# Optimization experiments

Measured on AMD Instinct MI355X. Metric: run time of the kernel, lower is better.

Reference implementation:

```python
import jax, jax.numpy as jnp
import numpy as np

B, T, D, L, H = 8, 1024, 768, 8, 12
BLOCK_SIZE = 4
HD = D // H


def setup_inputs() -> dict:
    key = jax.random.key(0)
    ks = jax.random.split(key, 10)
    sd = 0.02
    return {
        "x_init": jax.random.normal(ks[0], (B, T, D), jnp.float32),
        "attn_proj_w": jax.random.normal(ks[1], (L, D), jnp.float32) * sd,
        "mlp_proj_w": jax.random.normal(ks[2], (L, D), jnp.float32) * sd,
        "Wqkv": jax.random.normal(ks[3], (L, D, 3 * D), jnp.float32) * sd,
        "Wo": jax.random.normal(ks[4], (L, D, D), jnp.float32) * sd,
        "Wm1": jax.random.normal(ks[5], (L, D, 4 * D), jnp.float32) * sd,
        "Wm2": jax.random.normal(ks[6], (L, 4 * D, D), jnp.float32) * sd,
        "attn_scale": 1.0 + jax.random.normal(ks[7], (L, D), jnp.float32) * sd,
        "mlp_scale": 1.0 + jax.random.normal(ks[8], (L, D), jnp.float32) * sd,
        "ln_s": jnp.ones((L,), jnp.float32),
    }


def _rms_norm(x):
    # F.rms_norm with eps=None -> eps = finfo(dtype).eps
    eps = jnp.finfo(x.dtype).eps
    return x * jax.lax.rsqrt(jnp.mean(x * x, axis=-1, keepdims=True) + eps)


def _aggregate(V, q):
    # V: [n, B, T, D]; scalar-query depth attention (keys RMS-normed, values raw)
    K = _rms_norm(V)
    logits = jnp.einsum('d,nbtd->nbt', q, K)
    w = jax.nn.softmax(logits, axis=0)
    return jnp.einsum('nbt,nbtd->btd', w, V)


def _mha(x, wqkv, wo):
    # causal multi-head self-attention
    b, t, d = x.shape
    qkv = x @ wqkv                                   # [b, t, 3D]
    q, k, v = jnp.split(qkv, 3, axis=-1)
    q = q.reshape(b, t, H, HD)
    k = k.reshape(b, t, H, HD)
    v = v.reshape(b, t, H, HD)
    scores = jnp.einsum('bqhd,bkhd->bhqk', q, k) / np.sqrt(HD).astype(np.float32)
    mask = jnp.tril(jnp.ones((t, t), bool))
    scores = jnp.where(mask[None, None], scores, jnp.asarray(-1e30, scores.dtype))
    attn = jax.nn.softmax(scores, axis=-1)
    out = jnp.einsum('bhqk,bkhd->bqhd', attn, v).reshape(b, t, d)
    return out @ wo


def reference(x_init, attn_proj_w, mlp_proj_w, Wqkv, Wo, Wm1, Wm2,
              attn_scale, mlp_scale, ln_s):
    boundary_every = max(1, BLOCK_SIZE // 2)
    hist = [x_init]          # committed block representations
    partial = x_init         # intra-block partial accumulator
    for l in range(L):
        s = ln_s[l]
        V = jnp.stack(hist + [partial], axis=0)          # [n_hist+1, B, T, D]
        h = _aggregate(V, attn_proj_w[l])
        if l % boundary_every == 0:
            hist.append(partial)
            partial = jnp.zeros_like(partial)
        attn_out = _mha(_rms_norm(h) * s, Wqkv[l], Wo[l])
        partial = partial + attn_scale[l][None, None, :] * attn_out
        V2 = jnp.stack(hist + [partial], axis=0)
        h = _aggregate(V2, mlp_proj_w[l])
        mlp_out = jax.nn.gelu((_rms_norm(h) * s) @ Wm1[l]) @ Wm2[l]
        partial = partial + mlp_scale[l][None, None, :] * mlp_out
    return partial
```

## Files before the change

kernel.cpp:

```cpp
#include <hip/hip_runtime.h>
#include <hip/hip_bf16.h>
#include <math.h>
#include <stdint.h>

#define D_MODEL 768
#define T_SEQ   1024
#define B_BATCH 8
#define NHEAD   12
#define HDIM    64
#define NLAYER  8

typedef unsigned short u16;
typedef __attribute__((ext_vector_type(8))) short bf16x8;
typedef __attribute__((ext_vector_type(4))) float f32x4;
typedef __attribute__((ext_vector_type(4))) uint32_t u32x4;

static constexpr size_t BTD  = (size_t)B_BATCH * T_SEQ * D_MODEL;
static constexpr int    ROWS = B_BATCH * T_SEQ;
static constexpr float  EPSF = 1.1920928955078125e-07f;


__device__ __forceinline__ u16 f2bf(float x) {
    __hip_bfloat16 h = __float2bfloat16(x);
    return __builtin_bit_cast(u16, h);
}
__device__ __forceinline__ float bf2f(u16 u) {
    __hip_bfloat16 h = __builtin_bit_cast(__hip_bfloat16, u);
    return __bfloat162float(h);
}
__device__ __forceinline__ void split_bf(float x, u16& hi, u16& lo) {
    hi = f2bf(x);
    lo = f2bf(x - bf2f(hi));
}
__device__ __forceinline__ uint32_t cvt_pk_bf16(float a, float b) {
    uint32_t r;
    asm("v_cvt_pk_bf16_f32 %0, %1, %2" : "=v"(r) : "v"(a), "v"(b));
    return r;
}
__device__ __forceinline__ f32x4 mfma16(bf16x8 a, bf16x8 b, f32x4 c) {
    return __builtin_amdgcn_mfma_f32_16x16x32_bf16(a, b, c, 0, 0, 0);
}

__device__ __forceinline__ void gl_lds16(const void* g, void* l) {
    auto gp = reinterpret_cast<const __attribute__((address_space(1))) char*>(
        reinterpret_cast<uintptr_t>(g));
    auto lp = reinterpret_cast<__attribute__((address_space(3))) char*>(
        static_cast<uint32_t>(reinterpret_cast<uintptr_t>(l)));
    __builtin_amdgcn_global_load_lds(gp, lp, 16, 0, 0);
}

__device__ __forceinline__ float block_reduce_sum(float v, float* sbuf) {
    #pragma unroll
    for (int off = 32; off > 0; off >>= 1) v += __shfl_down(v, off);
    __syncthreads();
    if ((threadIdx.x & 63) == 0) sbuf[threadIdx.x >> 6] = v;
    __syncthreads();
    return sbuf[0] + sbuf[1] + sbuf[2] + sbuf[3];
}

__device__ __forceinline__ float gelu_fast(float x) {
    float z = 0.7978845608028654f * (x + 0.044715f * x * x * x);
    float e = __expf(2.f * z);
    return x - x / (e + 1.f);
}

template<int N>
__global__ __launch_bounds__(256)
void agg_norm_kernel(const float* __restrict__ v0, const float* __restrict__ v1,
                     const float* __restrict__ v2, const float* __restrict__ v3,
                     const float* __restrict__ v4,
                     const float* __restrict__ q,  const float* __restrict__ lns,
                     u16* __restrict__ xh) {
    __shared__ float sbuf[4];
    const float* V[5] = {v0, v1, v2, v3, v4};
    const size_t row = blockIdx.x;
    const int tid = threadIdx.x;

    float outv[3];
    if constexpr (N == 1) {
        #pragma unroll
        for (int j = 0; j < 3; ++j) outv[j] = v0[row * D_MODEL + tid + j * 256];
    } else {
        float qv[3];
        #pragma unroll
        for (int j = 0; j < 3; ++j) qv[j] = q[tid + j * 256];

        float vv[N][3];
        float logits[N];
        #pragma unroll
        for (int i = 0; i < N; ++i) {
            const float* vr = V[i] + row * D_MODEL;
            float ssq = 0.f, qd = 0.f;
            #pragma unroll
            for (int j = 0; j < 3; ++j) {
                float x = vr[tid + j * 256];
                vv[i][j] = x;
                ssq = fmaf(x, x, ssq);
                qd  = fmaf(qv[j], x, qd);
            }
            float S  = block_reduce_sum(ssq, sbuf);
            float Qd = block_reduce_sum(qd,  sbuf);
            logits[i] = Qd * rsqrtf(S * (1.f / 768.f) + EPSF);
        }
        float mx = logits[0];
        #pragma unroll
        for (int i = 1; i < N; ++i) mx = fmaxf(mx, logits[i]);
        float w[N];
        #pragma unroll
        for (int i = 0; i < N; ++i) w[i] = __expf(logits[i] - mx);
        w[0] *= 2.f;
        float wsum = 0.f;
        #pragma unroll
        for (int i = 0; i < N; ++i) wsum += w[i];
        float inv = 1.f / wsum;
        outv[0] = outv[1] = outv[2] = 0.f;
        #pragma unroll
        for (int i = 0; i < N; ++i) {
            float wi = w[i] * inv;
            #pragma unroll
            for (int j = 0; j < 3; ++j) outv[j] = fmaf(wi, vv[i][j], outv[j]);
        }
    }
    float ssq = 0.f;
    #pragma unroll
    for (int j = 0; j < 3; ++j) ssq = fmaf(outv[j], outv[j], ssq);
    float S2 = block_reduce_sum(ssq, sbuf);
    float scale = lns[0] * rsqrtf(S2 * (1.f / 768.f) + EPSF);
    #pragma unroll
    for (int j = 0; j < 3; ++j)
        xh[row * D_MODEL + tid + j * 256] = f2bf(outv[j] * scale);
}

__global__ __launch_bounds__(256)
void transpose_all(const float* __restrict__ Wqkv, const float* __restrict__ Wo,
                   const float* __restrict__ Wm1,  const float* __restrict__ Wm2,
                   u16* __restrict__ T0, u16* __restrict__ T1,
                   u16* __restrict__ T2, u16* __restrict__ T3) {
    const int id = blockIdx.x;
    const float* W; u16* Th; int K, N, t;
    if (id < 1728)      { W = Wqkv; Th = T0; K = 768;  N = 2304; t = id; }
    else if (id < 2304) { W = Wo;   Th = T1; K = 768;  N = 768;  t = id - 1728; }
    else if (id < 4608) { W = Wm1;  Th = T2; K = 768;  N = 3072; t = id - 2304; }
    else                { W = Wm2;  Th = T3; K = 3072; N = 768;  t = id - 4608; }
    const int nk = K >> 5;
    const int bk = (t % nk) * 32, bn = (t / nk) * 32;

    __shared__ float tt[32][33];
    const int r = threadIdx.x >> 3, c4 = (threadIdx.x & 7) * 4;
    float4 v = *(const float4*)&W[(size_t)(bk + r) * N + bn + c4];
    tt[r][c4 + 0] = v.x; tt[r][c4 + 1] = v.y; tt[r][c4 + 2] = v.z; tt[r][c4 + 3] = v.w;
    __syncthreads();
    u16 h[4];
    #pragma unroll
    for (int j = 0; j < 4; ++j) h[j] = f2bf(tt[c4 + j][r]);
    size_t o = (size_t)(bn + r) * K + bk + c4;
    *(uint2*)&Th[o] = make_uint2((uint32_t)h[0] | ((uint32_t)h[1] << 16),
                                 (uint32_t)h[2] | ((uint32_t)h[3] << 16));
}

__global__ __launch_bounds__(256)
void vt_transpose(const u16* __restrict__ vh, u16* __restrict__ vth) {
    __shared__ u16 th[32][36];
    const int bh = blockIdx.z;
    const int t0 = blockIdx.x * 32, d0 = blockIdx.y * 32;
    const int r = threadIdx.x >> 3, c = (threadIdx.x & 7) * 4;
    const size_t ib = ((size_t)(bh << 10) + t0 + r) * 64 + d0 + c;
    *(uint2*)&th[r][c] = *(const uint2*)&vh[ib];
    __syncthreads();
    const size_t ob = ((size_t)(bh << 6) + d0 + r) * 1024 + t0 + c;
    u16 a0 = th[c + 0][r], a1 = th[c + 1][r], a2 = th[c + 2][r], a3 = th[c + 3][r];
    *(uint2*)&vth[ob] = make_uint2((uint32_t)a0 | ((uint32_t)a1 << 16),
                                   (uint32_t)a2 | ((uint32_t)a3 << 16));
}

template<int EPI, int BN>
__global__ __launch_bounds__(256)
void gemm_bf1(const u16* __restrict__ Ah, const u16* __restrict__ Bh,
              float* __restrict__ Cf, u16* __restrict__ Ch,
              const float* __restrict__ scale, int M, int N, int K,
              u16* __restrict__ Qh, u16* __restrict__ Ql,
              u16* __restrict__ Kh, u16* __restrict__ Vh) {
    constexpr int NJ = BN / 32;
    constexpr int BUF_U16 = 4096 + BN * 32;
    __shared__ u16 smem[2 * BUF_U16];

    const int gx = gridDim.x, gy = gridDim.y;
    const int nwg = gx * gy;
    const int lin = blockIdx.y * gx + blockIdx.x;
    const int wg  = (lin & 7) * (nwg >> 3) + (lin >> 3);
    const int bn  = (wg % gx) * BN;
    const int bm  = (wg / gx) << 7;

    const int tid = threadIdx.x;
    const int w = tid >> 6, l = tid & 63;
    const int wr = w >> 1, wc = w & 1;

    const int grow = tid >> 2;
    const int gcol = (((tid & 3) ^ ((tid >> 3) & 3)) << 3);
    const size_t aoff0 = (size_t)(bm + grow) * K + gcol;
    const size_t boff0 = (size_t)(bn + grow) * K + gcol;
    const size_t s64 = (size_t)64 * K;
    char* sb0 = (char*)smem;
    char* sb1 = (char*)smem + 2 * BUF_U16;
    const uint32_t wq = (uint32_t)w << 10;

    auto stage = [&](char* sbuf, int k0) {
        gl_lds16(Ah + aoff0 + k0,       sbuf + 0    + wq);
        gl_lds16(Ah + aoff0 + s64 + k0, sbuf + 4096 + wq);
        gl_lds16(Bh + boff0 + k0,       sbuf + 8192 + wq);
        if constexpr (BN == 128)
            gl_lds16(Bh + boff0 + s64 + k0, sbuf + 12288 + wq);
    };

    f32x4 acc[4][NJ] = {};

    const int key8 = (((l & 15) >> 1) & 3) << 3;
    const int kswz = ((l >> 4) << 3) ^ key8;
    const int arow = wr * 64 + (l & 15);
    const int brow = wc * (BN / 2) + (l & 15);
    const int nk = K >> 5;

    stage(sb0, 0);
    for (int kt = 0; kt < nk; ++kt) {
        char* cur = (kt & 1) ? sb1 : sb0;
        char* nxt = (kt & 1) ? sb0 : sb1;
        if (kt + 1 < nk) {
            stage(nxt, (kt + 1) << 5);
            if constexpr (BN == 128)
                asm volatile("s_waitcnt vmcnt(4)\n\ts_barrier" ::: "memory");
            else
                asm volatile("s_waitcnt vmcnt(3)\n\ts_barrier" ::: "memory");
        } else {
            asm volatile("s_waitcnt vmcnt(0)\n\ts_barrier" ::: "memory");
        }
        __builtin_amdgcn_sched_barrier(0);

        const u16* bu = (const u16*)cur;
        bf16x8 ah[4], bh4[NJ];
        #pragma unroll
        for (int i = 0; i < 4; ++i)
            ah[i] = *(const bf16x8*)&bu[(arow + i * 16) * 32 + kswz];
        #pragma unroll
        for (int j = 0; j < NJ; ++j)
            bh4[j] = *(const bf16x8*)&bu[4096 + (brow + j * 16) * 32 + kswz];
        asm volatile("s_waitcnt lgkmcnt(0)" ::: "memory");
        __builtin_amdgcn_sched_barrier(0);
        asm volatile("s_barrier" ::: "memory");

        #pragma unroll
        for (int i = 0; i < 4; ++i) {
            #pragma unroll
            for (int j = 0; j < NJ; ++j)
                acc[i][j] = mfma16(ah[i], bh4[j], acc[i][j]);
        }
    }

    const int crow0 = bm + wr * 64 + ((l >> 4) << 2);
    const int ccol0 = bn + wc * (BN / 2) + (l & 15);
    #pragma unroll
    for (int i = 0; i < 4; ++i) {
        #pragma unroll
        for (int j = 0; j < NJ; ++j) {
            const int col = ccol0 + j * 16;
            #pragma unroll
            for (int r = 0; r < 4; ++r) {
                const int row = crow0 + i * 16 + r;
                const size_t o = (size_t)row * N + col;
                float v = acc[i][j][r];
                if (EPI == 1) {
                    Ch[o] = f2bf(gelu_fast(v));
                } else if (EPI == 2) {
                    Cf[o] += scale[col] * v;
                } else if (EPI == 4) {
                    Cf[o] = scale[col] * v;
                } else if (EPI == 3) {
                    const int which = (col >= 1536) ? 2 : ((col >= 768) ? 1 : 0);
                    const int hcol = col - which * 768;
                    const size_t dst = ((size_t)((row >> 10) * NHEAD + (hcol >> 6)) * 1024
                                        + (row & 1023)) * 64 + (hcol & 63);
                    if (which == 0) {
                        v *= 0.125f;
                        u16 hi, lo;
                        split_bf(v, hi, lo);
                        Qh[dst] = hi; Ql[dst] = lo;
                    } else if (which == 1) {
                        Kh[dst] = f2bf(v);
                    } else {
                        Vh[dst] = f2bf(v);
                    }
                }
            }
        }
    }
}

__global__ __launch_bounds__(256, 3)
void flash16(const u16* __restrict__ qh, const u16* __restrict__ ql,
             const u16* __restrict__ kh, const u16* __restrict__ vth,
             u16* __restrict__ ch) {
    const int id = blockIdx.x;
    const int r8 = id & 7, s = id >> 3;
    const int bh = r8 + 8 * (s >> 3);
    const int p  = s & 7;
    const int hh = bh % NHEAD, bb = bh / NHEAD;
    const int tid = threadIdx.x, w = tid >> 6, l = tid & 63;
    const int lq = l & 15, lg = l >> 4;
    const size_t hb = (size_t)bh << 16;

    const int wqA = p * 64 + w * 16;
    const int wqB = (15 - p) * 64 + w * 16;
    const int qA = wqA + lq, qB = wqB + lq;

    bf16x8 qA0, qA1, qA2, qA3, qB0, qB1, qB2, qB3;
    {
        const size_t qa = hb + ((size_t)qA << 6) + lg * 8;
        qA0 = *(const bf16x8*)(qh + qa);       qA1 = *(const bf16x8*)(ql + qa);
        qA2 = *(const bf16x8*)(qh + qa + 32);  qA3 = *(const bf16x8*)(ql + qa + 32);
        const size_t qb = hb + ((size_t)qB << 6) + lg * 8;
        qB0 = *(const bf16x8*)(qh + qb);       qB1 = *(const bf16x8*)(ql + qb);
        qB2 = *(const bf16x8*)(qh + qb + 32);  qB3 = *(const bf16x8*)(ql + qb + 32);
    }

    f32x4 oA[4] = {}, oB[4] = {};
    float mA = -30000.f, lsA = 0.f, mB = -30000.f, lsB = 0.f;
    const int ntiles = 32 - 2 * p;
    const int src0 = 32 * (lg & 1) + lq, src1 = src0 + 16;
    const bool hiHalf = lg >= 2;

    bf16x8 KA[4], KB[4], VA[4], VB[4];
    auto loadK = [&](bf16x8 (&K)[4], int k0) {
        const size_t kb0 = hb + (size_t)(k0 + lq) * 64 + lg * 8;
        const size_t kb1 = kb0 + 16 * 64;
        K[0] = *(const bf16x8*)(kh + kb0);
        K[1] = *(const bf16x8*)(kh + kb0 + 32);
        K[2] = *(const bf16x8*)(kh + kb1);
        K[3] = *(const bf16x8*)(kh + kb1 + 32);
    };
    auto loadV = [&](bf16x8 (&V)[4], int k0) {
        #pragma unroll
        for (int dt = 0; dt < 4; ++dt) {
            const size_t vb = hb + (size_t)(dt * 16 + lq) * 1024 + k0 + lg * 8;
            V[dt] = *(const bf16x8*)(vth + vb);
        }
    };

    auto path = [&](bf16x8 (&Kc)[4], bf16x8 (&vf)[4], int k0, int wqX, int qX,
                    bf16x8 q0, bf16x8 q1, bf16x8 q2, bf16x8 q3,
                    float& mX, float& lsX, f32x4 (&oX)[4]) {
        f32x4 s0 = {}, s1 = {};
        s0 = mfma16(Kc[0], q0, s0); s0 = mfma16(Kc[0], q1, s0);
        s0 = mfma16(Kc[1], q2, s0); s0 = mfma16(Kc[1], q3, s0);
        s1 = mfma16(Kc[2], q0, s1); s1 = mfma16(Kc[2], q1, s1);
        s1 = mfma16(Kc[3], q2, s1); s1 = mfma16(Kc[3], q3, s1);
        if (k0 + 31 > wqX) {
            #pragma unroll
            for (int r = 0; r < 4; ++r) {
                if (k0 + 4 * lg + r > qX)      s0[r] = -30000.f;
                if (k0 + 16 + 4 * lg + r > qX) s1[r] = -30000.f;
            }
        }
        float tmloc = fmaxf(fmaxf(fmaxf(s0[0], s0[1]), fmaxf(s0[2], s0[3])),
                            fmaxf(fmaxf(s1[0], s1[1]), fmaxf(s1[2], s1[3])));
        if (__any(tmloc > mX + 8.f)) {
            float tm = fmaxf(tmloc, __shfl_xor(tmloc, 16));
            tm = fmaxf(tm, __shfl_xor(tm, 32));
            const float mnew = fmaxf(mX, tm);
            const float fac = __expf(mX - mnew);
            mX = mnew;
            lsX *= fac;
            #pragma unroll
            for (int dt = 0; dt < 4; ++dt) {
                oX[dt][0] *= fac; oX[dt][1] *= fac;
                oX[dt][2] *= fac; oX[dt][3] *= fac;
            }
        }
        float ps = 0.f;
        #pragma unroll
        for (int r = 0; r < 4; ++r) {
            s0[r] = __expf(s0[r] - mX); ps += s0[r];
            s1[r] = __expf(s1[r] - mX); ps += s1[r];
        }
        lsX += ps;
        const uint32_t wA0 = cvt_pk_bf16(s0[0], s0[1]);
        const uint32_t wA1 = cvt_pk_bf16(s0[2], s0[3]);
        const uint32_t wB0 = cvt_pk_bf16(s1[0], s1[1]);
        const uint32_t wB1 = cvt_pk_bf16(s1[2], s1[3]);
        const uint32_t a0 = (uint32_t)__shfl((int)wA0, src0);
        const uint32_t b0 = (uint32_t)__shfl((int)wB0, src0);
        const uint32_t a1 = (uint32_t)__shfl((int)wA1, src0);
        const uint32_t b1 = (uint32_t)__shfl((int)wB1, src0);
        const uint32_t a2 = (uint32_t)__shfl((int)wA0, src1);
        const uint32_t b2 = (uint32_t)__shfl((int)wB0, src1);
        const uint32_t a3 = (uint32_t)__shfl((int)wA1, src1);
        const uint32_t b3 = (uint32_t)__shfl((int)wB1, src1);
        u32x4 pw = { hiHalf ? b0 : a0, hiHalf ? b1 : a1,
                     hiHalf ? b2 : a2, hiHalf ? b3 : a3 };
        const bf16x8 pb = __builtin_bit_cast(bf16x8, pw);
        #pragma unroll
        for (int dt = 0; dt < 4; ++dt)
            oX[dt] = mfma16(vf[dt], pb, oX[dt]);
    };

    auto step = [&](bf16x8 (&Kc)[4], bf16x8 (&Vc)[4],
                    bf16x8 (&Kn)[4], bf16x8 (&Vn)[4], int kt) {
        const int k0 = kt * 32;
        const int ktn = (kt + 1 < ntiles) ? kt + 1 : kt;
        loadK(Kn, ktn * 32);
        loadV(Vn, ktn * 32);
        if (k0 <= wqB + 15)
            path(Kc, Vc, k0, wqB, qB, qB0, qB1, qB2, qB3, mB, lsB, oB);
        if (k0 <= wqA + 15)
            path(Kc, Vc, k0, wqA, qA, qA0, qA1, qA2, qA3, mA, lsA, oA);
    };

    loadK(KA, 0);
    loadV(VA, 0);
    for (int kt = 0; kt < ntiles; kt += 2) {
        step(KA, VA, KB, VB, kt);
        step(KB, VB, KA, VA, kt + 1);
    }

    lsA += __shfl_xor(lsA, 16); lsA += __shfl_xor(lsA, 32);
    lsB += __shfl_xor(lsB, 16); lsB += __shfl_xor(lsB, 32);
    const float invA = 1.f / lsA, invB = 1.f / lsB;
    const size_t cbA = ((size_t)(bb * 1024 + qA)) * 768 + hh * 64;
    const size_t cbB = ((size_t)(bb * 1024 + qB)) * 768 + hh * 64;
    #pragma unroll
    for (int dt = 0; dt < 4; ++dt) {
        u16 h4[4];
        #pragma unroll
        for (int r = 0; r < 4; ++r) h4[r] = f2bf(oA[dt][r] * invA);
        size_t co = cbA + dt * 16 + 4 * lg;
        *(uint2*)&ch[co] = make_uint2((uint32_t)h4[0] | ((uint32_t)h4[1] << 16),
                                      (uint32_t)h4[2] | ((uint32_t)h4[3] << 16));
        #pragma unroll
        for (int r = 0; r < 4; ++r) h4[r] = f2bf(oB[dt][r] * invB);
        co = cbB + dt * 16 + 4 * lg;
        *(uint2*)&ch[co] = make_uint2((uint32_t)h4[0] | ((uint32_t)h4[1] << 16),
                                      (uint32_t)h4[2] | ((uint32_t)h4[3] << 16));
    }
}


extern "C" void kernel_launch(void* const* d_in, const int* in_sizes, int n_in,
                              void* d_out, int out_size, void* d_ws, size_t ws_size,
                              hipStream_t stream) {
    const float* x0     = (const float*)d_in[0];
    const float* aproj  = (const float*)d_in[1];
    const float* mproj  = (const float*)d_in[2];
    const float* Wqkv   = (const float*)d_in[3];
    const float* Wo     = (const float*)d_in[4];
    const float* Wm1    = (const float*)d_in[5];
    const float* Wm2    = (const float*)d_in[6];
    const float* ascale = (const float*)d_in[7];
    const float* mscale = (const float*)d_in[8];
    const float* lns    = (const float*)d_in[9];
    float* out = (float*)d_out;
    char*  base = (char*)d_ws;

    float* p1  = (float*)base;
    float* p2  = p1 + BTD;
    float* p3  = p2 + BTD;
    u16*   xnh = (u16*)(base + 12 * BTD);
    u16*   wt0 = (u16*)(base + 14 * BTD);
    u16*   wt1 = wt0 + (size_t)2304 * 768;
    u16*   wt2 = wt1 + (size_t)768 * 768;
    u16*   wt3 = wt2 + (size_t)3072 * 768;
    char*  QB  = (char*)(wt3 + (size_t)768 * 3072);
    u16* qh   = (u16*)QB;
    u16* ql   = qh  + BTD;
    u16* kh   = ql  + BTD;
    u16* vh   = kh  + BTD;
    u16* vth  = vh  + BTD;
    u16* ctxh = vh;
    u16* midh = qh;

    float* pb[3] = {p1, p2, p3};
    const float* L[5] = {x0, nullptr, nullptr, nullptr, nullptr};
    int nL = 1;
    float* partial_w = nullptr;
    int pidx = 0;

    auto launch_agg = [&](const float* qvec, const float* lnsl) {
        const float* a = L[0];
        const float* b = (nL > 1) ? L[1] : nullptr;
        const float* c = (nL > 2) ? L[2] : nullptr;
        const float* d = (nL > 3) ? L[3] : nullptr;
        const float* e = (nL > 4) ? L[4] : nullptr;
        switch (nL) {
        case 1: agg_norm_kernel<1><<<dim3(ROWS), 256, 0, stream>>>(a, b, c, d, e, qvec, lnsl, xnh); break;
        case 2: agg_norm_kernel<2><<<dim3(ROWS), 256, 0, stream>>>(a, b, c, d, e, qvec, lnsl, xnh); break;
        case 3: agg_norm_kernel<3><<<dim3(ROWS), 256, 0, stream>>>(a, b, c, d, e, qvec, lnsl, xnh); break;
        case 4: agg_norm_kernel<4><<<dim3(ROWS), 256, 0, stream>>>(a, b, c, d, e, qvec, lnsl, xnh); break;
        default: agg_norm_kernel<5><<<dim3(ROWS), 256, 0, stream>>>(a, b, c, d, e, qvec, lnsl, xnh); break;
        }
    };

    for (int l = 0; l < NLAYER; ++l) {
        transpose_all<<<dim3(6912), 256, 0, stream>>>(
            Wqkv + (size_t)l * D_MODEL * 3 * D_MODEL,
            Wo   + (size_t)l * D_MODEL * D_MODEL,
            Wm1  + (size_t)l * D_MODEL * 4 * D_MODEL,
            Wm2  + (size_t)l * 4 * D_MODEL * D_MODEL,
            wt0, wt1, wt2, wt3);

        launch_agg(aproj + (size_t)l * D_MODEL, lns + l);

        const bool boundary = ((l & 1) == 0);
        if (boundary) {
            float* np = (pidx < 3) ? pb[pidx] : out;
            ++pidx;
            partial_w = np;
            L[nL++] = np;
        }

        gemm_bf1<3, 128><<<dim3(3 * D_MODEL / 128, ROWS / 128), 256, 0, stream>>>(
            xnh, wt0, nullptr, nullptr, nullptr,
            ROWS, 3 * D_MODEL, D_MODEL, qh, ql, kh, vh);

        vt_transpose<<<dim3(T_SEQ / 32, HDIM / 32, B_BATCH * NHEAD), 256, 0, stream>>>(
            vh, vth);

        flash16<<<dim3(768), 256, 0, stream>>>(qh, ql, kh, vth, ctxh);

        if (boundary)
            gemm_bf1<4, 64><<<dim3(D_MODEL / 64, ROWS / 128), 256, 0, stream>>>(
                ctxh, wt1, partial_w, nullptr,
                ascale + (size_t)l * D_MODEL, ROWS, D_MODEL, D_MODEL,
                nullptr, nullptr, nullptr, nullptr);
        else
            gemm_bf1<2, 64><<<dim3(D_MODEL / 64, ROWS / 128), 256, 0, stream>>>(
                ctxh, wt1, partial_w, nullptr,
                ascale + (size_t)l * D_MODEL, ROWS, D_MODEL, D_MODEL,
                nullptr, nullptr, nullptr, nullptr);

        launch_agg(mproj + (size_t)l * D_MODEL, lns + l);

        gemm_bf1<1, 128><<<dim3(4 * D_MODEL / 128, ROWS / 128), 256, 0, stream>>>(
            xnh, wt2, nullptr, midh,
            nullptr, ROWS, 4 * D_MODEL, D_MODEL,
            nullptr, nullptr, nullptr, nullptr);
        gemm_bf1<2, 64><<<dim3(D_MODEL / 64, ROWS / 128), 256, 0, stream>>>(
            midh, wt3, partial_w, nullptr,
            mscale + (size_t)l * D_MODEL, ROWS, D_MODEL, 4 * D_MODEL,
            nullptr, nullptr, nullptr, nullptr);
    }
}
```

Measured before the change: 2.778 ms.

## Split paired-tile flash attention blocks into single-tile blocks with higher occupancy

The causal flash-attention kernel previously had each block handle two complementary query tiles (p and 15-p) to balance work. Now each block handles one 64-row query tile, with twice as many blocks, alternating short and long tiles in launch order, and launch bounds raised to 6 blocks per SIMD group. V is now loaded per step instead of double-buffered, which cuts register use. This trades load balance within a block and K/V reuse across two query tiles for more occupancy and parallelism, and it exposes the V load latency.

```diff
diff --git a/kernel.cpp b/kernel.cpp
--- a/kernel.cpp
+++ b/kernel.cpp
@@ -294,40 +294,37 @@
     }
 }
 
-__global__ __launch_bounds__(256, 3)
+__global__ __launch_bounds__(256, 6)
 void flash16(const u16* __restrict__ qh, const u16* __restrict__ ql,
              const u16* __restrict__ kh, const u16* __restrict__ vth,
              u16* __restrict__ ch) {
     const int id = blockIdx.x;
     const int r8 = id & 7, s = id >> 3;
-    const int bh = r8 + 8 * (s >> 3);
-    const int p  = s & 7;
+    const int bh = r8 + 8 * (s >> 4);
+    const int t4 = s & 15;
+    const int tile = (t4 & 1) ? (15 - (t4 >> 1)) : (t4 >> 1);
     const int hh = bh % NHEAD, bb = bh / NHEAD;
     const int tid = threadIdx.x, w = tid >> 6, l = tid & 63;
     const int lq = l & 15, lg = l >> 4;
     const size_t hb = (size_t)bh << 16;
 
-    const int wqA = p * 64 + w * 16;
-    const int wqB = (15 - p) * 64 + w * 16;
-    const int qA = wqA + lq, qB = wqB + lq;
-
-    bf16x8 qA0, qA1, qA2, qA3, qB0, qB1, qB2, qB3;
+    const int wq = tile * 64 + w * 16;
+    const int q = wq + lq;
+
+    bf16x8 qf0, qf1, qf2, qf3;
     {
-        const size_t qa = hb + ((size_t)qA << 6) + lg * 8;
-        qA0 = *(const bf16x8*)(qh + qa);       qA1 = *(const bf16x8*)(ql + qa);
-        qA2 = *(const bf16x8*)(qh + qa + 32);  qA3 = *(const bf16x8*)(ql + qa + 32);
-        const size_t qb = hb + ((size_t)qB << 6) + lg * 8;
-        qB0 = *(const bf16x8*)(qh + qb);       qB1 = *(const bf16x8*)(ql + qb);
-        qB2 = *(const bf16x8*)(qh + qb + 32);  qB3 = *(const bf16x8*)(ql + qb + 32);
-    }
-
-    f32x4 oA[4] = {}, oB[4] = {};
-    float mA = -30000.f, lsA = 0.f, mB = -30000.f, lsB = 0.f;
-    const int ntiles = 32 - 2 * p;
+        const size_t qa = hb + ((size_t)q << 6) + lg * 8;
+        qf0 = *(const bf16x8*)(qh + qa);       qf1 = *(const bf16x8*)(ql + qa);
+        qf2 = *(const bf16x8*)(qh + qa + 32);  qf3 = *(const bf16x8*)(ql + qa + 32);
+    }
+
+    f32x4 o[4] = {};
+    float m = -30000.f, ls = 0.f;
+    const int ntiles = 2 * tile + 2;
     const int src0 = 32 * (lg & 1) + lq, src1 = src0 + 16;
     const bool hiHalf = lg >= 2;
 
-    bf16x8 KA[4], KB[4], VA[4], VB[4];
+    bf16x8 KA[4], KB[4];
     auto loadK = [&](bf16x8 (&K)[4], int k0) {
         const size_t kb0 = hb + (size_t)(k0 + lq) * 64 + lg * 8;
         const size_t kb1 = kb0 + 16 * 64;
@@ -344,43 +341,41 @@
         }
     };
 
-    auto path = [&](bf16x8 (&Kc)[4], bf16x8 (&vf)[4], int k0, int wqX, int qX,
-                    bf16x8 q0, bf16x8 q1, bf16x8 q2, bf16x8 q3,
-                    float& mX, float& lsX, f32x4 (&oX)[4]) {
+    auto path = [&](bf16x8 (&Kc)[4], bf16x8 (&vf)[4], int k0) {
         f32x4 s0 = {}, s1 = {};
-        s0 = mfma16(Kc[0], q0, s0); s0 = mfma16(Kc[0], q1, s0);
-        s0 = mfma16(Kc[1], q2, s0); s0 = mfma16(Kc[1], q3, s0);
-        s1 = mfma16(Kc[2], q0, s1); s1 = mfma16(Kc[2], q1, s1);
-        s1 = mfma16(Kc[3], q2, s1); s1 = mfma16(Kc[3], q3, s1);
-        if (k0 + 31 > wqX) {
+        s0 = mfma16(Kc[0], qf0, s0); s0 = mfma16(Kc[0], qf1, s0);
+        s0 = mfma16(Kc[1], qf2, s0); s0 = mfma16(Kc[1], qf3, s0);
+        s1 = mfma16(Kc[2], qf0, s1); s1 = mfma16(Kc[2], qf1, s1);
+        s1 = mfma16(Kc[3], qf2, s1); s1 = mfma16(Kc[3], qf3, s1);
+        if (k0 + 31 > wq) {
             #pragma unroll
             for (int r = 0; r < 4; ++r) {
-                if (k0 + 4 * lg + r > qX)      s0[r] = -30000.f;
-                if (k0 + 16 + 4 * lg + r > qX) s1[r] = -30000.f;
+                if (k0 + 4 * lg + r > q)      s0[r] = -30000.f;
+                if (k0 + 16 + 4 * lg + r > q) s1[r] = -30000.f;
             }
         }
         float tmloc = fmaxf(fmaxf(fmaxf(s0[0], s0[1]), fmaxf(s0[2], s0[3])),
                             fmaxf(fmaxf(s1[0], s1[1]), fmaxf(s1[2], s1[3])));
-        if (__any(tmloc > mX + 8.f)) {
+        if (__any(tmloc > m + 8.f)) {
             float tm = fmaxf(tmloc, __shfl_xor(tmloc, 16));
             tm = fmaxf(tm, __shfl_xor(tm, 32));
-            const float mnew = fmaxf(mX, tm);
-            const float fac = __expf(mX - mnew);
-            mX = mnew;
-            lsX *= fac;
+            const float mnew = fmaxf(m, tm);
+            const float fac = __expf(m - mnew);
+            m = mnew;
+            ls *= fac;
             #pragma unroll
             for (int dt = 0; dt < 4; ++dt) {
-                oX[dt][0] *= fac; oX[dt][1] *= fac;
-                oX[dt][2] *= fac; oX[dt][3] *= fac;
+                o[dt][0] *= fac; o[dt][1] *= fac;
+                o[dt][2] *= fac; o[dt][3] *= fac;
             }
         }
         float ps = 0.f;
         #pragma unroll
         for (int r = 0; r < 4; ++r) {
-            s0[r] = __expf(s0[r] - mX); ps += s0[r];
-            s1[r] = __expf(s1[r] - mX); ps += s1[r];
-        }
-        lsX += ps;
+            s0[r] = __expf(s0[r] - m); ps += s0[r];
+            s1[r] = __expf(s1[r] - m); ps += s1[r];
+        }
+        ls += ps;
         const uint32_t wA0 = cvt_pk_bf16(s0[0], s0[1]);
         const uint32_t wA1 = cvt_pk_bf16(s0[2], s0[3]);
         const uint32_t wB0 = cvt_pk_bf16(s1[0], s1[1]);
@@ -398,44 +393,34 @@
         const bf16x8 pb = __builtin_bit_cast(bf16x8, pw);
         #pragma unroll
         for (int dt = 0; dt < 4; ++dt)
-            oX[dt] = mfma16(vf[dt], pb, oX[dt]);
+            o[dt] = mfma16(vf[dt], pb, o[dt]);
     };
 
-    auto step = [&](bf16x8 (&Kc)[4], bf16x8 (&Vc)[4],
-                    bf16x8 (&Kn)[4], bf16x8 (&Vn)[4], int kt) {
+    auto step = [&](bf16x8 (&Kc)[4], bf16x8 (&Kn)[4], int kt) {
         const int k0 = kt * 32;
+        bf16x8 vf[4];
+        loadV(vf, k0);
         const int ktn = (kt + 1 < ntiles) ? kt + 1 : kt;
         loadK(Kn, ktn * 32);
-        loadV(Vn, ktn * 32);
-        if (k0 <= wqB + 15)
-            path(Kc, Vc, k0, wqB, qB, qB0, qB1, qB2, qB3, mB, lsB, oB);
-        if (k0 <= wqA + 15)
-            path(Kc, Vc, k0, wqA, qA, qA0, qA1, qA2, qA3, mA, lsA, oA);
+        if (k0 <= wq + 15)
+            path(Kc, vf, k0);
     };
 
     loadK(KA, 0);
-    loadV(VA, 0);
     for (int kt = 0; kt < ntiles; kt += 2) {
-        step(KA, VA, KB, VB, kt);
-        step(KB, VB, KA, VA, kt + 1);
-    }
-
-    lsA += __shfl_xor(lsA, 16); lsA += __shfl_xor(lsA, 32);
-    lsB += __shfl_xor(lsB, 16); lsB += __shfl_xor(lsB, 32);
-    const float invA = 1.f / lsA, invB = 1.f / lsB;
-    const size_t cbA = ((size_t)(bb * 1024 + qA)) * 768 + hh * 64;
-    const size_t cbB = ((size_t)(bb * 1024 + qB)) * 768 + hh * 64;
+        step(KA, KB, kt);
+        step(KB, KA, kt + 1);
+    }
+
+    ls += __shfl_xor(ls, 16); ls += __shfl_xor(ls, 32);
+    const float inv = 1.f / ls;
+    const size_t cb = ((size_t)(bb * 1024 + q)) * 768 + hh * 64;
     #pragma unroll
     for (int dt = 0; dt < 4; ++dt) {
         u16 h4[4];
         #pragma unroll
-        for (int r = 0; r < 4; ++r) h4[r] = f2bf(oA[dt][r] * invA);
-        size_t co = cbA + dt * 16 + 4 * lg;
-        *(uint2*)&ch[co] = make_uint2((uint32_t)h4[0] | ((uint32_t)h4[1] << 16),
-                                      (uint32_t)h4[2] | ((uint32_t)h4[3] << 16));
-        #pragma unroll
-        for (int r = 0; r < 4; ++r) h4[r] = f2bf(oB[dt][r] * invB);
-        co = cbB + dt * 16 + 4 * lg;
+        for (int r = 0; r < 4; ++r) h4[r] = f2bf(o[dt][r] * inv);
+        const size_t co = cb + dt * 16 + 4 * lg;
         *(uint2*)&ch[co] = make_uint2((uint32_t)h4[0] | ((uint32_t)h4[1] << 16),
                                       (uint32_t)h4[2] | ((uint32_t)h4[3] << 16));
     }
@@ -521,7 +506,7 @@
         vt_transpose<<<dim3(T_SEQ / 32, HDIM / 32, B_BATCH * NHEAD), 256, 0, stream>>>(
             vh, vth);
 
-        flash16<<<dim3(768), 256, 0, stream>>>(qh, ql, kh, vth, ctxh);
+        flash16<<<dim3(1536), 256, 0, stream>>>(qh, ql, kh, vth, ctxh);
 
         if (boundary)
             gemm_bf1<4, 64><<<dim3(D_MODEL / 64, ROWS / 128), 256, 0, stream>>>(
```

New measurement: 4.838 ms. +74.2%, slower.
